# Optimization experiments

Measured on AMD Instinct MI355X. Metric: run time of the kernel, lower is better.

Reference implementation:

```python
import jax, jax.numpy as jnp
import numpy as np

B, T, D, H = 4, 2048, 1024, 16
HD = D // H  # 64


def setup_inputs() -> dict:
    key = jax.random.key(0)
    ks = jax.random.split(key, 9)
    s = 1.0 / np.sqrt(D)
    return {
        "x": jax.random.normal(ks[0], (B, T, D), dtype=jnp.float32),
        "Wq": jax.random.uniform(ks[1], (D, D), jnp.float32, -s, s),
        "bq": jax.random.uniform(ks[2], (D,), jnp.float32, -s, s),
        "Wk": jax.random.uniform(ks[3], (D, D), jnp.float32, -s, s),
        "bk": jax.random.uniform(ks[4], (D,), jnp.float32, -s, s),
        "Wv": jax.random.uniform(ks[5], (D, D), jnp.float32, -s, s),
        "bv": jax.random.uniform(ks[6], (D,), jnp.float32, -s, s),
        "Wp": jax.random.uniform(ks[7], (D, D), jnp.float32, -s, s),
        "bp": jax.random.uniform(ks[8], (D,), jnp.float32, -s, s),
    }


def reference(x, Wq, bq, Wk, bk, Wv, bv, Wp, bp):
    b, t, _ = x.shape
    # project and split heads: (B, H, T, HD)
    def heads(w, bias):
        y = x @ w + bias
        return y.reshape(b, t, H, HD).transpose(0, 2, 1, 3)
    q = heads(Wq, bq)
    k = heads(Wk, bk)
    v = heads(Wv, bv)
    scores = jnp.einsum('bhqd,bhkd->bhqk', q, k) / np.sqrt(HD)
    causal = jnp.tril(jnp.ones((t, t), dtype=bool))
    scores = jnp.where(causal, scores, -jnp.inf)
    attn = jax.nn.softmax(scores, axis=-1)  # dropout p=0 -> identity
    out = jnp.einsum('bhqk,bhkd->bhqd', attn, v)
    out = out.transpose(0, 2, 1, 3).reshape(b, t, D)
    return out @ Wp + bp
```

## Files before the change

kernel.cpp:

```cpp
#include <hip/hip_runtime.h>
#include <hip/hip_bf16.h>
#include <stdint.h>

#define B_ 4
#define T_ 2048
#define D_ 1024
#define H_ 16
#define HD_ 64
#define M_TOT (B_ * T_)

typedef unsigned short u16t;
typedef __bf16 bf16x4 __attribute__((ext_vector_type(4)));
typedef __bf16 bf16x8 __attribute__((ext_vector_type(8)));
typedef float f32x4 __attribute__((ext_vector_type(4)));
typedef float f32x16 __attribute__((ext_vector_type(16)));

__device__ __forceinline__ u16t f2bf(float f) {
    union { float f; uint32_t u; } x; x.f = f;
    uint32_t r = x.u + 0x7fffu + ((x.u >> 16) & 1u);
    return (u16t)(r >> 16);
}

__device__ __forceinline__ float fexp2(float x) { return __builtin_amdgcn_exp2f(x); }

__device__ __forceinline__ void gload16(const void* g, void* l) {
    __builtin_amdgcn_global_load_lds((const __attribute__((address_space(1))) void*)g,
                                     (__attribute__((address_space(3))) void*)l, 16, 0, 0);
}

__global__ __launch_bounds__(256) void prep_kernel(const float* __restrict__ x,
                                                   const float* __restrict__ W0,
                                                   const float* __restrict__ W1,
                                                   const float* __restrict__ W2,
                                                   const float* __restrict__ W3,
                                                   u16t* __restrict__ xb,
                                                   u16t* __restrict__ T0,
                                                   u16t* __restrict__ T1,
                                                   u16t* __restrict__ T2,
                                                   u16t* __restrict__ T3) {
    __shared__ u16t tile[64][65];
    const int z = blockIdx.z;
    const int t = threadIdx.x;
    if (z >= 4) {
        int bid = (z - 4) * 256 + blockIdx.y * 16 + blockIdx.x;
        int i = bid * 256 + t;
        const float4* p = (const float4*)x + (size_t)i * 2;
        float4 a = p[0], b = p[1];
        u16t o[8] = {f2bf(a.x), f2bf(a.y), f2bf(a.z), f2bf(a.w),
                     f2bf(b.x), f2bf(b.y), f2bf(b.z), f2bf(b.w)};
        *(uint4*)(xb + (size_t)i * 8) = *(const uint4*)o;
        return;
    }
    const float* W; u16t* To;
    switch (z) {
        case 0: W = W0; To = T0; break;
        case 1: W = W1; To = T1; break;
        case 2: W = W2; To = T2; break;
        default: W = W3; To = T3; break;
    }
    int n0 = blockIdx.x * 64, k0 = blockIdx.y * 64;
#pragma unroll
    for (int i = 0; i < 16; ++i) {
        int idx = i * 256 + t;
        int r = idx >> 6, c = idx & 63;
        tile[r][c] = f2bf(W[(size_t)(k0 + r) * D_ + n0 + c]);
    }
    __syncthreads();
#pragma unroll
    for (int i = 0; i < 16; ++i) {
        int idx = i * 256 + t;
        int r = idx >> 6, c = idx & 63;
        To[(size_t)(n0 + r) * D_ + k0 + c] = tile[c][r];
    }
}

__global__ __launch_bounds__(256) void gemm_qkv_kernel(const u16t* __restrict__ A,
                                                       const u16t* __restrict__ Wt3,
                                                       const float* __restrict__ bq,
                                                       const float* __restrict__ bk,
                                                       const float* __restrict__ bv,
                                                       u16t* __restrict__ qo,
                                                       u16t* __restrict__ ko,
                                                       u16t* __restrict__ vto,
                                                       float qscale) {
    __shared__ u16t As[128 * 64];
    __shared__ u16t Bs[128 * 64];
    const int t = threadIdx.x;
    const int lane = t & 63, w = t >> 6;
    const int wm = w >> 1, wn = w & 1;
    const int l15 = lane & 15, l4 = lane >> 4;
    const int m0 = blockIdx.x * 128;
    const int n0g = blockIdx.y * 128;
    const int K = D_;

    f32x4 acc[4][4] = {};

    for (int k0 = 0; k0 < K; k0 += 64) {
#pragma unroll
        for (int i = 0; i < 4; ++i) {
            int lin = i * 256 + t;
            int r = lin >> 3, c = (lin & 7) * 8;
            int ldsoff = (i * 256 + w * 64) * 8;
            gload16(&A[(size_t)(m0 + r) * K + k0 + c], &As[ldsoff]);
            gload16(&Wt3[(size_t)(n0g + r) * K + k0 + c], &Bs[ldsoff]);
        }
        __syncthreads();
#pragma unroll
        for (int ks = 0; ks < 64; ks += 32) {
            bf16x8 af[4], bf[4];
#pragma unroll
            for (int i = 0; i < 4; ++i) {
                af[i] = *(const bf16x8*)&As[(wm * 64 + i * 16 + l15) * 64 + ks + l4 * 8];
                bf[i] = *(const bf16x8*)&Bs[(wn * 64 + i * 16 + l15) * 64 + ks + l4 * 8];
            }
#pragma unroll
            for (int mi = 0; mi < 4; ++mi)
#pragma unroll
                for (int ni = 0; ni < 4; ++ni)
                    acc[mi][ni] = __builtin_amdgcn_mfma_f32_16x16x32_bf16(
                        af[mi], bf[ni], acc[mi][ni], 0, 0, 0);
        }
        __syncthreads();
    }

    const int sel = blockIdx.y >> 3;
    const int n0 = (blockIdx.y & 7) * 128;
    const float* bias = sel == 0 ? bq : (sel == 1 ? bk : bv);
    const float scale = sel == 0 ? qscale : 1.0f;

#pragma unroll
    for (int mi = 0; mi < 4; ++mi) {
#pragma unroll
        for (int ni = 0; ni < 4; ++ni) {
            int col = n0 + wn * 64 + ni * 16 + l15;
            float bn = bias[col];
            if (sel < 2) {
                u16t* outp = sel == 0 ? qo : ko;
#pragma unroll
                for (int r = 0; r < 4; ++r) {
                    int row = m0 + wm * 64 + mi * 16 + l4 * 4 + r;
                    outp[(size_t)row * D_ + col] = f2bf((acc[mi][ni][r] + bn) * scale);
                }
            } else {
                int token0 = m0 + wm * 64 + mi * 16 + l4 * 4;
                u16t o4[4];
#pragma unroll
                for (int r = 0; r < 4; ++r) o4[r] = f2bf(acc[mi][ni][r] + bn);
                int b = token0 >> 11, tb = token0 & (T_ - 1);
                int h = col >> 6, hd = col & 63;
                *(uint2*)&vto[(((size_t)b * H_ + h) * HD_ + hd) * T_ + tb] = *(const uint2*)o4;
            }
        }
    }
}

__global__ __launch_bounds__(256) void gemm_proj_kernel(const u16t* __restrict__ A,
                                                        const u16t* __restrict__ Wt,
                                                        const float* __restrict__ bias,
                                                        float* __restrict__ outp) {
    __shared__ u16t As[128 * 64];
    __shared__ u16t Bs[128 * 64];
    const int t = threadIdx.x;
    const int lane = t & 63, w = t >> 6;
    const int wm = w >> 1, wn = w & 1;
    const int l15 = lane & 15, l4 = lane >> 4;
    const int m0 = blockIdx.x * 128, n0 = blockIdx.y * 128;
    const int K = D_, N = D_;

    f32x4 acc[4][4] = {};

    for (int k0 = 0; k0 < K; k0 += 64) {
#pragma unroll
        for (int i = 0; i < 4; ++i) {
            int lin = i * 256 + t;
            int r = lin >> 3, c = (lin & 7) * 8;
            int ldsoff = (i * 256 + w * 64) * 8;
            gload16(&A[(size_t)(m0 + r) * K + k0 + c], &As[ldsoff]);
            gload16(&Wt[(size_t)(n0 + r) * K + k0 + c], &Bs[ldsoff]);
        }
        __syncthreads();
#pragma unroll
        for (int ks = 0; ks < 64; ks += 32) {
            bf16x8 af[4], bf[4];
#pragma unroll
            for (int i = 0; i < 4; ++i) {
                af[i] = *(const bf16x8*)&As[(wm * 64 + i * 16 + l15) * 64 + ks + l4 * 8];
                bf[i] = *(const bf16x8*)&Bs[(wn * 64 + i * 16 + l15) * 64 + ks + l4 * 8];
            }
#pragma unroll
            for (int mi = 0; mi < 4; ++mi)
#pragma unroll
                for (int ni = 0; ni < 4; ++ni)
                    acc[mi][ni] = __builtin_amdgcn_mfma_f32_16x16x32_bf16(
                        af[mi], bf[ni], acc[mi][ni], 0, 0, 0);
        }
        __syncthreads();
    }

#pragma unroll
    for (int mi = 0; mi < 4; ++mi) {
#pragma unroll
        for (int ni = 0; ni < 4; ++ni) {
            int col = n0 + wn * 64 + ni * 16 + l15;
            float bn = bias[col];
#pragma unroll
            for (int r = 0; r < 4; ++r) {
                int row = m0 + wm * 64 + mi * 16 + l4 * 4 + r;
                outp[(size_t)row * N + col] = acc[mi][ni][r] + bn;
            }
        }
    }
}

__global__ __launch_bounds__(256) void attn_kernel(const u16t* __restrict__ Q,
                                                   const u16t* __restrict__ K,
                                                   const u16t* __restrict__ Vt,
                                                   u16t* __restrict__ O) {
    __shared__ u16t smem[16384];

    const int t = threadIdx.x;
    const int lane = t & 63, w = t >> 6;
    const int l31 = lane & 31, l5 = lane >> 5;

    const int lin = blockIdx.x;
    const int bh = lin & 63;
    const int q_idx = lin >> 6;
    const int hi = q_idx >> 2, lo = q_idx & 3;
    const int qtile = ((0x348F >> (hi * 4)) & 15) ^ ((0x2130 >> (lo * 4)) & 15);

    const size_t base = (size_t)(bh >> 4) * T_ * D_ + (size_t)(bh & 15) * HD_;
    const size_t vtbase = (size_t)bh * HD_ * T_;
    const int q0 = qtile * 128;
    const int qsub0 = q0 + w * 32;
    const int sw = l31 & 7;

    const int sr = t >> 3, sc16 = t & 7;
    const int g16 = sc16 ^ (sr & 7);
    const u16t* kp = &K[base + (size_t)sr * D_ + g16 * 8];
    const u16t* vp = &Vt[vtbase + (size_t)sr * T_ + g16 * 8];

    auto stage = [&](int jt, int buf) {
        const u16t* kq = kp + (size_t)jt * 64 * D_;
        const u16t* vq = vp + (size_t)jt * 64;
        u16t* kd = smem + buf * 4096;
        u16t* vd = smem + 8192 + buf * 4096;
#pragma unroll
        for (int c = 0; c < 2; ++c) {
            gload16(kq + (size_t)c * 32 * D_, kd + c * 2048 + w * 512);
            gload16(vq + (size_t)c * 32 * T_, vd + c * 2048 + w * 512);
        }
    };

    const u16t* qp = &Q[base + (size_t)(qsub0 + l31) * D_ + l5 * 8];
    bf16x8 qf[4];
#pragma unroll
    for (int ks = 0; ks < 4; ++ks) qf[ks] = *(const bf16x8*)&qp[ks * 16];

    f32x16 acc_oT[2] = {};
    float lrun = 0.f;

    const int njt = 2 * qtile + 2;
    stage(0, 0);

    for (int jt = 0; jt < njt; ++jt) {
        const int cur = jt & 1;
        const int kv0 = jt * 64;
        __syncthreads();
        if (jt + 1 < njt) stage(jt + 1, cur ^ 1);

        if (kv0 <= qsub0 + 31) {
            const u16t* kb = smem + cur * 4096;
            const u16t* vb = smem + 8192 + cur * 4096;

            f32x16 accs[2] = {};
            __builtin_amdgcn_s_setprio(1);
#pragma unroll
            for (int half = 0; half < 2; ++half) {
                const u16t* kr = kb + (half * 32 + l31) * 64;
#pragma unroll
                for (int ks = 0; ks < 4; ++ks) {
                    bf16x8 kf = *(const bf16x8*)&kr[((ks * 2 + l5) ^ sw) * 8];
                    accs[half] = __builtin_amdgcn_mfma_f32_32x32x16_bf16(
                        kf, qf[ks], accs[half], 0, 0, 0);
                }
            }
            __builtin_amdgcn_s_setprio(0);

            const int qrow = qsub0 + l31;
            if (kv0 + 63 > qsub0) {
#pragma unroll
                for (int half = 0; half < 2; ++half)
#pragma unroll
                    for (int r = 0; r < 16; ++r) {
                        int kv = kv0 + half * 32 + (r & 3) + 8 * (r >> 2) + 4 * l5;
                        if (kv > qrow) accs[half][r] = -1e30f;
                    }
            }

            float ps[4] = {0.f, 0.f, 0.f, 0.f};
            bf16x8 pb[4];
#pragma unroll
            for (int half = 0; half < 2; ++half)
#pragma unroll
                for (int r = 0; r < 16; ++r) {
                    float p = fexp2(accs[half][r]);
                    ps[r & 3] += p;
                    pb[half * 2 + (r >> 3)][r & 7] = (__bf16)p;
                }
            lrun += (ps[0] + ps[1]) + (ps[2] + ps[3]);

            __builtin_amdgcn_s_setprio(1);
#pragma unroll
            for (int dh = 0; dh < 2; ++dh) {
                const u16t* vr = vb + (dh * 32 + l31) * 64;
#pragma unroll
                for (int m = 0; m < 4; ++m) {
                    int g = 2 * (m & 1) + 4 * (m >> 1);
                    bf16x4 v0 = *(const bf16x4*)&vr[((g ^ sw) << 3) + 4 * l5];
                    bf16x4 v1 = *(const bf16x4*)&vr[(((g + 1) ^ sw) << 3) + 4 * l5];
                    bf16x8 af = __builtin_shufflevector(v0, v1, 0, 1, 2, 3, 4, 5, 6, 7);
                    acc_oT[dh] = __builtin_amdgcn_mfma_f32_32x32x16_bf16(
                        af, pb[m], acc_oT[dh], 0, 0, 0);
                }
            }
            __builtin_amdgcn_s_setprio(0);
        }
    }

    lrun += __shfl_xor(lrun, 32);
    __syncthreads();
    float inv = __builtin_amdgcn_rcpf(lrun);
    u16t* ot = smem + w * 2304;
#pragma unroll
    for (int dh = 0; dh < 2; ++dh)
#pragma unroll
        for (int r = 0; r < 16; ++r) {
            int d = dh * 32 + (r & 3) + 8 * (r >> 2) + 4 * l5;
            ot[l31 * 72 + d] = f2bf(acc_oT[dh][r] * inv);
        }
    __syncthreads();
#pragma unroll
    for (int p = 0; p < 4; ++p) {
        int idx = p * 64 + lane;
        int row = idx >> 3, c8 = (idx & 7) * 8;
        *(uint4*)&O[base + (size_t)(qsub0 + row) * D_ + c8] = *(const uint4*)&ot[row * 72 + c8];
    }
}

extern "C" void kernel_launch(void* const* d_in, const int* in_sizes, int n_in,
                              void* d_out, int out_size, void* d_ws, size_t ws_size,
                              hipStream_t stream) {
    const float* x  = (const float*)d_in[0];
    const float* Wq = (const float*)d_in[1];
    const float* bq = (const float*)d_in[2];
    const float* Wk = (const float*)d_in[3];
    const float* bk = (const float*)d_in[4];
    const float* Wv = (const float*)d_in[5];
    const float* bv = (const float*)d_in[6];
    const float* Wp = (const float*)d_in[7];
    const float* bp = (const float*)d_in[8];
    float* out = (float*)d_out;

    u16t* ws = (u16t*)d_ws;
    const size_t XN = (size_t)M_TOT * D_;
    u16t* xb  = ws;
    u16t* q   = ws + XN;
    u16t* k   = ws + 2 * XN;
    u16t* vt  = ws + 3 * XN;
    u16t* wtq = ws + 4 * XN;
    u16t* wtk = wtq + (size_t)D_ * D_;
    u16t* wtv = wtk + (size_t)D_ * D_;
    u16t* wtp = wtv + (size_t)D_ * D_;
    u16t* o   = xb;

    prep_kernel<<<dim3(16, 16, 20), 256, 0, stream>>>(x, Wq, Wk, Wv, Wp,
                                                      xb, wtq, wtk, wtv, wtp);

    gemm_qkv_kernel<<<dim3(64, 24), 256, 0, stream>>>(
        xb, wtq, bq, bk, bv, q, k, vt, 0.125f * 1.44269504088896f);

    attn_kernel<<<dim3(1024), 256, 0, stream>>>(q, k, vt, o);

    gemm_proj_kernel<<<dim3(64, 8), 256, 0, stream>>>(o, wtp, bp, out);
}
```

Baseline: 176.7 us.

## Double-buffer LDS tiles and XOR-swizzle layout in QKV and projection GEMMs

```diff
diff --git a/kernel.cpp b/kernel.cpp
--- a/kernel.cpp
+++ b/kernel.cpp
@@ -83,35 +83,39 @@
                                                        u16t* __restrict__ ko,
                                                        u16t* __restrict__ vto,
                                                        float qscale) {
-    __shared__ u16t As[128 * 64];
-    __shared__ u16t Bs[128 * 64];
+    __shared__ u16t smem[32768];
     const int t = threadIdx.x;
     const int lane = t & 63, w = t >> 6;
     const int wm = w >> 1, wn = w & 1;
     const int l15 = lane & 15, l4 = lane >> 4;
     const int m0 = blockIdx.x * 128;
     const int n0g = blockIdx.y * 128;
-    const int K = D_;
+
+    const int sr = t >> 3, sc8 = t & 7;
+    const int sg = (sc8 ^ (sr & 7)) * 8;
+
+    auto stageg = [&](int k0, int bufoff) {
+#pragma unroll
+        for (int i = 0; i < 4; ++i) {
+            int r = (i * 256 + t) >> 3;
+            int ldsoff = bufoff + (i * 256 + w * 64) * 8;
+            gload16(&A[(size_t)(m0 + r) * D_ + k0 + sg], &smem[ldsoff]);
+            gload16(&Wt3[(size_t)(n0g + r) * D_ + k0 + sg], &smem[16384 + ldsoff]);
+        }
+    };
 
     f32x4 acc[4][4] = {};
 
-    for (int k0 = 0; k0 < K; k0 += 64) {
-#pragma unroll
-        for (int i = 0; i < 4; ++i) {
-            int lin = i * 256 + t;
-            int r = lin >> 3, c = (lin & 7) * 8;
-            int ldsoff = (i * 256 + w * 64) * 8;
-            gload16(&A[(size_t)(m0 + r) * K + k0 + c], &As[ldsoff]);
-            gload16(&Wt3[(size_t)(n0g + r) * K + k0 + c], &Bs[ldsoff]);
-        }
-        __syncthreads();
+    auto compute = [&](int bufoff) {
 #pragma unroll
         for (int ks = 0; ks < 64; ks += 32) {
             bf16x8 af[4], bf[4];
 #pragma unroll
             for (int i = 0; i < 4; ++i) {
-                af[i] = *(const bf16x8*)&As[(wm * 64 + i * 16 + l15) * 64 + ks + l4 * 8];
-                bf[i] = *(const bf16x8*)&Bs[(wn * 64 + i * 16 + l15) * 64 + ks + l4 * 8];
+                int row = i * 16 + l15;
+                int g = (((ks >> 3) + l4) ^ (l15 & 7)) * 8;
+                af[i] = *(const bf16x8*)&smem[bufoff + (wm * 64 + row) * 64 + g];
+                bf[i] = *(const bf16x8*)&smem[16384 + bufoff + (wn * 64 + row) * 64 + g];
             }
 #pragma unroll
             for (int mi = 0; mi < 4; ++mi)
@@ -120,7 +124,16 @@
                     acc[mi][ni] = __builtin_amdgcn_mfma_f32_16x16x32_bf16(
                         af[mi], bf[ni], acc[mi][ni], 0, 0, 0);
         }
+    };
+
+    stageg(0, 0);
+    for (int kk = 0; kk < 16; kk += 2) {
         __syncthreads();
+        stageg((kk + 1) * 64, 8192);
+        compute(0);
+        __syncthreads();
+        if (kk + 2 < 16) stageg((kk + 2) * 64, 0);
+        compute(8192);
     }
 
     const int sel = blockIdx.y >> 3;
@@ -158,34 +171,38 @@
                                                         const u16t* __restrict__ Wt,
                                                         const float* __restrict__ bias,
                                                         float* __restrict__ outp) {
-    __shared__ u16t As[128 * 64];
-    __shared__ u16t Bs[128 * 64];
+    __shared__ u16t smem[32768];
     const int t = threadIdx.x;
     const int lane = t & 63, w = t >> 6;
     const int wm = w >> 1, wn = w & 1;
     const int l15 = lane & 15, l4 = lane >> 4;
     const int m0 = blockIdx.x * 128, n0 = blockIdx.y * 128;
-    const int K = D_, N = D_;
+
+    const int sr = t >> 3, sc8 = t & 7;
+    const int sg = (sc8 ^ (sr & 7)) * 8;
+
+    auto stageg = [&](int k0, int bufoff) {
+#pragma unroll
+        for (int i = 0; i < 4; ++i) {
+            int r = (i * 256 + t) >> 3;
+            int ldsoff = bufoff + (i * 256 + w * 64) * 8;
+            gload16(&A[(size_t)(m0 + r) * D_ + k0 + sg], &smem[ldsoff]);
+            gload16(&Wt[(size_t)(n0 + r) * D_ + k0 + sg], &smem[16384 + ldsoff]);
+        }
+    };
 
     f32x4 acc[4][4] = {};
 
-    for (int k0 = 0; k0 < K; k0 += 64) {
-#pragma unroll
-        for (int i = 0; i < 4; ++i) {
-            int lin = i * 256 + t;
-            int r = lin >> 3, c = (lin & 7) * 8;
-            int ldsoff = (i * 256 + w * 64) * 8;
-            gload16(&A[(size_t)(m0 + r) * K + k0 + c], &As[ldsoff]);
-            gload16(&Wt[(size_t)(n0 + r) * K + k0 + c], &Bs[ldsoff]);
-        }
-        __syncthreads();
+    auto compute = [&](int bufoff) {
 #pragma unroll
         for (int ks = 0; ks < 64; ks += 32) {
             bf16x8 af[4], bf[4];
 #pragma unroll
             for (int i = 0; i < 4; ++i) {
-                af[i] = *(const bf16x8*)&As[(wm * 64 + i * 16 + l15) * 64 + ks + l4 * 8];
-                bf[i] = *(const bf16x8*)&Bs[(wn * 64 + i * 16 + l15) * 64 + ks + l4 * 8];
+                int row = i * 16 + l15;
+                int g = (((ks >> 3) + l4) ^ (l15 & 7)) * 8;
+                af[i] = *(const bf16x8*)&smem[bufoff + (wm * 64 + row) * 64 + g];
+                bf[i] = *(const bf16x8*)&smem[16384 + bufoff + (wn * 64 + row) * 64 + g];
             }
 #pragma unroll
             for (int mi = 0; mi < 4; ++mi)
@@ -194,7 +211,16 @@
                     acc[mi][ni] = __builtin_amdgcn_mfma_f32_16x16x32_bf16(
                         af[mi], bf[ni], acc[mi][ni], 0, 0, 0);
         }
+    };
+
+    stageg(0, 0);
+    for (int kk = 0; kk < 16; kk += 2) {
         __syncthreads();
+        stageg((kk + 1) * 64, 8192);
+        compute(0);
+        __syncthreads();
+        if (kk + 2 < 16) stageg((kk + 2) * 64, 0);
+        compute(8192);
     }
 
 #pragma unroll
@@ -206,7 +232,7 @@
 #pragma unroll
             for (int r = 0; r < 4; ++r) {
                 int row = m0 + wm * 64 + mi * 16 + l4 * 4 + r;
-                outp[(size_t)row * N + col] = acc[mi][ni][r] + bn;
+                outp[(size_t)row * D_ + col] = acc[mi][ni][r] + bn;
             }
         }
     }
```

Result: faster. 151.7 us (median of 2 runs) (-14.2%).
